# Kernel optimization log

Hardware: AMD Instinct MI355X
Metric: run time of the kernel (lower is better)

The kernel has to match this reference:

```python
import jax, jax.numpy as jnp
import numpy as np

B, L, D = 2, 2048, 768
HID = 32           # saliency gate hidden dim
WINDOWS = (8, 32)  # sorted window sizes
CLAMP_MIN, CLAMP_MAX = 0.05, 0.95
SCALE = 1.0 / np.sqrt(D)  # memory_dim == d_model


def setup_inputs() -> dict:
    key = jax.random.key(0)
    ks = jax.random.split(key, 16)
    s = 0.02
    return {
        "hidden_states": jax.random.normal(ks[0], (B, L, D), jnp.float32),
        "saliency_scores": jax.random.uniform(ks[1], (B, L), jnp.float32),
        # SaliencyGate MLP: Linear(1->HID), SiLU, Linear(HID->D)
        "gw1": jax.random.normal(ks[2], (HID, 1), jnp.float32) * s,
        "gb1": jnp.zeros((HID,), jnp.float32),
        "gw2": jax.random.normal(ks[3], (D, HID), jnp.float32) * s,
        "gb2": jnp.zeros((D,), jnp.float32),
        # SelectiveMemory projections
        "wq": jax.random.normal(ks[4], (D, D), jnp.float32) * s,
        "bq": jnp.zeros((D,), jnp.float32),
        "wk": jax.random.normal(ks[5], (D, D), jnp.float32) * s,
        "bk": jnp.zeros((D,), jnp.float32),
        "wv": jax.random.normal(ks[6], (D, D), jnp.float32) * s,
        "bv": jnp.zeros((D,), jnp.float32),
        "wo": jax.random.normal(ks[7], (D, D), jnp.float32) * s,
        "bo": jnp.zeros((D,), jnp.float32),
    }


def _forward(hidden_states, saliency_scores, gw1, gb1, gw2, gb2,
             wq, bq, wk, bk, wv, bv, wo, bo):
    # ---- SaliencyGate: scalar score -> MLP -> sigmoid gate -> clamp ----
    s = saliency_scores[..., None]                          # (b, l, 1)
    h1 = jax.nn.silu(s @ gw1.T + gb1)                       # (b, l, HID)
    gates = jax.nn.sigmoid(h1 @ gw2.T + gb2)                # (b, l, D)
    gates = jnp.clip(gates, CLAMP_MIN, CLAMP_MAX)
    h = hidden_states * gates

    # ---- SelectiveMemory: multi-window local attention ----
    q = h @ wq.T + bq                                       # (b, l, D)
    k = h @ wk.T + bk
    v = h @ wv.T + bv
    # Torch pads hidden_states with zeros before k/v projection; linear of a
    # zero row equals the bias, so padded key/value rows are exactly bk / bv.
    contexts = []
    for w in WINDOWS:
        kp = jnp.concatenate(
            [jnp.broadcast_to(bk, (B, w - 1, D)), k], axis=1)  # (b, l+w-1, D)
        vp = jnp.concatenate(
            [jnp.broadcast_to(bv, (B, w - 1, D)), v], axis=1)
        idx = jnp.arange(L)[:, None] + jnp.arange(w)[None, :]  # (l, w)
        kw = kp[:, idx]                                        # (b, l, w, D)
        vw = vp[:, idx]
        scores = jnp.einsum('bld,blwd->blw', q, kw) * SCALE
        attn = jax.nn.softmax(scores, axis=-1)
        contexts.append(jnp.einsum('blw,blwd->bld', attn, vw))
    merged = (contexts[0] + contexts[1]) * 0.5 if len(contexts) > 1 else contexts[0]
    return h + merged @ wo.T + bo


def reference(hidden_states, saliency_scores, gw1, gb1, gw2, gb2,
              wq, bq, wk, bk, wv, bv, wo, bo):
    return _forward(hidden_states, saliency_scores, gw1, gb1, gw2, gb2,
                    wq, bq, wk, bk, wv, bv, wo, bo)
```

## Files before the change

### kernel.cpp

```cpp
#include <hip/hip_runtime.h>
#include <hip/hip_bf16.h>
#include <stdint.h>

#define Bb 2
#define Ll 2048
#define Dd 768
#define HID 32
#define BL (Bb*Ll)
#define KPAD 32
#define KROWS (KPAD+Ll+16)

typedef __hip_bfloat16 bf16;
typedef __attribute__((ext_vector_type(8))) short short8;
typedef __attribute__((ext_vector_type(4))) short short4s;
typedef __attribute__((ext_vector_type(4))) float floatx4;

__device__ __forceinline__ float b2f(short u) {
    union { float f; unsigned i; } x; x.i = ((unsigned)(unsigned short)u) << 16; return x.f;
}
__device__ __forceinline__ bf16 f2b(float x) { return __float2bfloat16(x); }
__device__ __forceinline__ short f2bs(float x) {
    bf16 t = __float2bfloat16(x);
    union { bf16 h; short s; } u; u.h = t; return u.s;
}

typedef __attribute__((address_space(1))) const unsigned int guint;
typedef __attribute__((address_space(3))) unsigned int luint;
__device__ __forceinline__ void gload16(const bf16* g, bf16* l) {
    __builtin_amdgcn_global_load_lds((guint*)g, (luint*)l, 16, 0, 0);
}

#define CONV_VB 2304
#define KP_VB   (Bb*48)
#define VT_VB   ((Bb*Dd*48)/256)
#define PREP_VB (CONV_VB+KP_VB+VT_VB)
#define GATE_VB (BL/8)
__global__ __launch_bounds__(256) void prep_gate_kernel(
        const float* __restrict__ wq, const float* __restrict__ wk,
        const float* __restrict__ wv, const float* __restrict__ wo,
        const float* __restrict__ bk, const float* __restrict__ bv,
        const float* __restrict__ hidden, const float* __restrict__ sal,
        const float* __restrict__ gw1, const float* __restrict__ gb1,
        const float* __restrict__ gw2, const float* __restrict__ gb2,
        bf16* __restrict__ wout, bf16* __restrict__ kp, bf16* __restrict__ vT,
        bf16* __restrict__ h_b) {
    __shared__ bf16 g2t[32 * 770];
    __shared__ float h1s[8][HID];
    int bx = blockIdx.x, tid = threadIdx.x;
    if (bx < CONV_VB) {
        int idx = bx * 256 + tid;
        const int per = Dd * Dd / 4;
        int w = idx / per, r = idx % per;
        const float* src = (w == 0) ? wq : (w == 1) ? wk : (w == 2) ? wv : wo;
        float4 v = reinterpret_cast<const float4*>(src)[r];
        bf16* o = wout + (size_t)w * Dd * Dd + (size_t)r * 4;
        o[0] = f2b(v.x); o[1] = f2b(v.y); o[2] = f2b(v.z); o[3] = f2b(v.w);
    } else if (bx < CONV_VB + KP_VB) {
        int pb = bx - CONV_VB;
        int b = pb / 48, c = pb % 48;
        int row = (c < 32) ? c : (KPAD + Ll + (c - 32));
        size_t base = ((size_t)b * KROWS + row) * Dd;
        for (int i = tid; i < Dd; i += 256)
            kp[base + i] = (c < 32) ? f2b(bk[i]) : f2b(0.f);
    } else if (bx < PREP_VB) {
        int o = (bx - CONV_VB - KP_VB) * 256 + tid;
        int b = o / (Dd * 48); int rem = o - b * Dd * 48;
        int n = rem / 48, c = rem % 48;
        int col = (c < 32) ? c : (KPAD + Ll + (c - 32));
        vT[((size_t)b * Dd + n) * KROWS + col] = (c < 32) ? f2b(bv[n]) : f2b(0.f);
    } else {
        int row0 = (bx - PREP_VB) * 8;
#pragma unroll
        for (int k2 = 0; k2 < 24; ++k2) {
            int o4 = tid + k2 * 256;
            float4 v = reinterpret_cast<const float4*>(gw2)[o4];
            int d = o4 >> 3, j = (o4 & 7) * 4;
            g2t[(j + 0) * 770 + d] = f2b(v.x);
            g2t[(j + 1) * 770 + d] = f2b(v.y);
            g2t[(j + 2) * 770 + d] = f2b(v.z);
            g2t[(j + 3) * 770 + d] = f2b(v.w);
        }
        {
            int rr = tid >> 5, j = tid & 31;
            float s = sal[row0 + rr];
            float x = s * gw1[j] + gb1[j];
            h1s[rr][j] = x / (1.f + __expf(-x));
        }
        __syncthreads();
#pragma unroll
        for (int dl = 0; dl < 3; ++dl) {
            int d = tid + dl * 256;
            float base = gb2[d];
            float acc[8];
#pragma unroll
            for (int rr = 0; rr < 8; ++rr) acc[rr] = base;
#pragma unroll
            for (int j = 0; j < HID; ++j) {
                float wj = b2f(*(const short*)&g2t[j * 770 + d]);
#pragma unroll
                for (int rr = 0; rr < 8; ++rr) acc[rr] += h1s[rr][j] * wj;
            }
#pragma unroll
            for (int rr = 0; rr < 8; ++rr) {
                float g = 1.f / (1.f + __expf(-acc[rr]));
                g = fminf(fmaxf(g, 0.05f), 0.95f);
                size_t off = (size_t)(row0 + rr) * Dd + d;
                h_b[off] = f2b(hidden[off] * g);
            }
        }
    }
}

template<int NF, int BK>
__device__ __forceinline__ void gemm_core(const bf16* __restrict__ Ag, const bf16* __restrict__ Wg,
                                          int m0, int n0, bf16* As, bf16* Bs,
                                          floatx4 (&acc)[4][NF]) {
    const int tid  = threadIdx.x;
    const int wave = tid >> 6, lane = tid & 63;
    const int lrow = lane & 15, koff = (lane >> 4) * 8;
    const int wm = (wave >> 1) * 64, wn = (wave & 1) * (NF * 16);
    const int RS = BK * 2;
    const char* Asb = (const char*)As;
    const char* Bsb = (const char*)Bs;

    for (int k0 = 0; k0 < Dd; k0 += BK) {
#pragma unroll
        for (int c = 0; c < BK / 16; ++c) {
            int p = tid * 16 + c * 4096;
            int r = p / RS;
            int o = (p % RS) ^ ((r & 7) << 4);
            gload16(Ag + (size_t)(m0 + r) * Dd + k0 + (o >> 1),
                    As + (wave * 1024 + c * 4096) / 2);
        }
#pragma unroll
        for (int c = 0; c < NF * BK / 64; ++c) {
            int p = tid * 16 + c * 4096;
            int r = p / RS;
            int o = (p % RS) ^ ((r & 7) << 4);
            gload16(Wg + (size_t)(n0 + r) * Dd + k0 + (o >> 1),
                    Bs + (wave * 1024 + c * 4096) / 2);
        }
        __syncthreads();
#pragma unroll
        for (int kk = 0; kk < BK; kk += 32) {
            short8 a[4], b[NF];
#pragma unroll
            for (int i = 0; i < 4; ++i) {
                int row = wm + i * 16 + lrow;
                int byt = row * RS + (((kk + koff) * 2) ^ ((row & 7) << 4));
                a[i] = *reinterpret_cast<const short8*>(Asb + byt);
            }
#pragma unroll
            for (int j = 0; j < NF; ++j) {
                int row = wn + j * 16 + lrow;
                int byt = row * RS + (((kk + koff) * 2) ^ ((row & 7) << 4));
                b[j] = *reinterpret_cast<const short8*>(Bsb + byt);
            }
#pragma unroll
            for (int i = 0; i < 4; ++i)
#pragma unroll
                for (int j = 0; j < NF; ++j)
                    acc[i][j] = __builtin_amdgcn_mfma_f32_16x16x32_bf16(a[i], b[j], acc[i][j], 0, 0, 0);
        }
        __syncthreads();
    }
}

__global__ __launch_bounds__(256, 2) void gemm_qkv(
        const bf16* __restrict__ A, const bf16* __restrict__ W3,
        const float* __restrict__ bq, const float* __restrict__ bk, const float* __restrict__ bv,
        bf16* __restrict__ qo, bf16* __restrict__ kp, bf16* __restrict__ vT) {
    __shared__ bf16 As[128 * 128];
    __shared__ bf16 Bs[128 * 128];
    int bid = blockIdx.x;
    int xcd = bid & 7, idx = bid >> 3;
    int mtile = (xcd >> 1) * 8 + (idx & 7);
    int ntile = (xcd & 1) * 9 + (idx >> 3);
    int tgt = ntile / 6;
    int n0 = (ntile % 6) * 128;
    int m0 = mtile * 128;
    const bf16* W = W3 + (size_t)tgt * Dd * Dd;
    const float* bias = (tgt == 0) ? bq : (tgt == 1) ? bk : bv;

    floatx4 acc[4][4] = {};
    gemm_core<4, 128>(A, W, m0, n0, As, Bs, acc);

    int wave = threadIdx.x >> 6, lane = threadIdx.x & 63;
    int wm = (wave >> 1) * 64, wn = (wave & 1) * 64;
    int crow = (lane >> 4) * 4, ccol = lane & 15;
#pragma unroll
    for (int i = 0; i < 4; ++i)
#pragma unroll
        for (int j = 0; j < 4; ++j) {
            int n = n0 + wn + j * 16 + ccol;
            float bb = bias[n];
            int m = m0 + wm + i * 16 + crow;
            int b_ = m >> 11, l = m & 2047;
            if (tgt == 2) {
                short4s pk;
#pragma unroll
                for (int rr = 0; rr < 4; ++rr) pk[rr] = f2bs(acc[i][j][rr] + bb);
                *reinterpret_cast<short4s*>(vT + ((size_t)b_ * Dd + n) * KROWS + KPAD + l) = pk;
            } else {
#pragma unroll
                for (int rr = 0; rr < 4; ++rr) {
                    size_t orow = (tgt == 0) ? (size_t)(m + rr)
                                             : ((size_t)b_ * KROWS + KPAD + l + rr);
                    bf16* outp = (tgt == 0) ? qo : kp;
                    outp[orow * Dd + n] = f2b(acc[i][j][rr] + bb);
                }
            }
        }
}

__global__ __launch_bounds__(256, 2) void gemm_out(
        const bf16* __restrict__ A, const bf16* __restrict__ W,
        const float* __restrict__ bias, const bf16* __restrict__ addend,
        float* __restrict__ out) {
    __shared__ bf16 As[128 * 64];
    __shared__ bf16 Bs[64 * 64];
    int bid = blockIdx.x;
    int xcd = bid & 7, idx = bid >> 3;
    int mtile = (xcd >> 1) * 8 + (idx & 7);
    int ntile = (xcd & 1) * 6 + (idx >> 3);
    int n0 = ntile * 64, m0 = mtile * 128;

    floatx4 acc[4][2] = {};
    gemm_core<2, 64>(A, W, m0, n0, As, Bs, acc);

    int wave = threadIdx.x >> 6, lane = threadIdx.x & 63;
    int wm = (wave >> 1) * 64, wn = (wave & 1) * 32;
    int crow = (lane >> 4) * 4, ccol = lane & 15;
#pragma unroll
    for (int i = 0; i < 4; ++i)
#pragma unroll
        for (int j = 0; j < 2; ++j) {
            int n = n0 + wn + j * 16 + ccol;
            float bb = bias[n];
#pragma unroll
            for (int rr = 0; rr < 4; ++rr) {
                int m = m0 + wm + i * 16 + crow + rr;
                size_t o = (size_t)m * Dd + n;
                out[o] = acc[i][j][rr] + bb + b2f(*(const short*)(addend + o));
            }
        }
}

#define AW 8
__global__ __launch_bounds__(512) void attn_kernel(
        const bf16* __restrict__ q, const bf16* __restrict__ kp, const bf16* __restrict__ vT,
        bf16* __restrict__ merged) {
    __shared__ float Sp[AW][16][66];
    __shared__ bf16 wlds[AW][16 * 64];
    const int tid = threadIdx.x;
    const int wv = tid >> 6, lane = tid & 63;
    const int bid = blockIdx.x;
    const int g = (bid & 7) * 32 + (bid >> 3);
    const int b = g >> 7, L0 = (g & 127) * 16;
    const int lrow = lane & 15, koff = (lane >> 4) * 8;
    const int crow = (lane >> 4) * 4, ccol = lane & 15;
    const float scale = 0.03608439182435161f;

    const bf16* qbase = q  + ((size_t)(b * Ll + L0 + lrow)) * Dd + koff + wv * 96;
    const bf16* kbase = kp + ((size_t)b * KROWS + L0 + lrow) * Dd + koff + wv * 96;
    floatx4 s4[4] = {};
#pragma unroll
    for (int ks = 0; ks < 3; ++ks) {
        short8 a = *reinterpret_cast<const short8*>(qbase + ks * 32);
#pragma unroll
        for (int f = 0; f < 4; ++f) {
            short8 bb = *reinterpret_cast<const short8*>(kbase + (size_t)f * 16 * Dd + ks * 32);
            s4[f] = __builtin_amdgcn_mfma_f32_16x16x32_bf16(a, bb, s4[f], 0, 0, 0);
        }
    }
#pragma unroll
    for (int f = 0; f < 4; ++f)
#pragma unroll
        for (int rr = 0; rr < 4; ++rr)
            Sp[wv][crow + rr][f * 16 + ccol] = s4[f][rr];
    __syncthreads();

#pragma unroll
    for (int rr = 0; rr < 4; ++rr) {
        int r = crow + rr;
        float z[4], e[4];
#pragma unroll
        for (int f = 0; f < 4; ++f) {
            int j = f * 16 + ccol;
            float v = 0.f;
#pragma unroll
            for (int w = 0; w < AW; ++w) v += Sp[w][r][j];
            bool valid = (j >= r + 1) && (j <= r + 32);
            z[f] = valid ? v * scale : -3.0e38f;
        }
        float m = fmaxf(fmaxf(z[0], z[1]), fmaxf(z[2], z[3]));
#pragma unroll
        for (int off = 1; off < 16; off <<= 1) m = fmaxf(m, __shfl_xor(m, off));
        float S32 = 0.f, S8 = 0.f;
#pragma unroll
        for (int f = 0; f < 4; ++f) {
            e[f] = __expf(z[f] - m);
            S32 += e[f];
            int j = f * 16 + ccol;
            S8 += ((j >= r + 25) && (j <= r + 32)) ? e[f] : 0.f;
        }
#pragma unroll
        for (int off = 1; off < 16; off <<= 1) {
            S32 += __shfl_xor(S32, off);
            S8  += __shfl_xor(S8, off);
        }
        float i32 = 0.5f / S32, i8 = 0.5f / S8;
#pragma unroll
        for (int f = 0; f < 4; ++f) {
            int j = f * 16 + ccol;
            float wgt = e[f] * i32 + (((j >= r + 25) && (j <= r + 32)) ? e[f] * i8 : 0.f);
            int byt = ((r * 64 + j) * 2) ^ ((r & 7) << 4);
            *reinterpret_cast<bf16*>(reinterpret_cast<char*>(wlds[wv]) + byt) = f2b(wgt);
        }
    }

    short8 wa[2];
#pragma unroll
    for (int ks = 0; ks < 2; ++ks) {
        int byt = ((lrow * 64 + ks * 32 + koff) * 2) ^ ((lrow & 7) << 4);
        wa[ks] = *reinterpret_cast<const short8*>(reinterpret_cast<const char*>(wlds[wv]) + byt);
    }
    const bf16* vbase = vT + (size_t)b * Dd * KROWS + L0;
    bf16* obase = merged + ((size_t)(b * Ll + L0 + ccol)) * Dd;
#pragma unroll
    for (int fn = 0; fn < 6; ++fn) {
        int nr = wv * 96 + fn * 16;
        floatx4 acc = {};
#pragma unroll
        for (int ks = 0; ks < 2; ++ks) {
            short8 bb = *reinterpret_cast<const short8*>(vbase + (size_t)(nr + lrow) * KROWS + ks * 32 + koff);
            acc = __builtin_amdgcn_mfma_f32_16x16x32_bf16(bb, wa[ks], acc, 0, 0, 0);
        }
        short4s pk;
#pragma unroll
        for (int rr = 0; rr < 4; ++rr) pk[rr] = f2bs(acc[rr]);
        *reinterpret_cast<short4s*>(obase + nr + crow) = pk;
    }
}

extern "C" void kernel_launch(void* const* d_in, const int* in_sizes, int n_in,
                              void* d_out, int out_size, void* d_ws, size_t ws_size,
                              hipStream_t stream) {
    const float* hidden = (const float*)d_in[0];
    const float* sal    = (const float*)d_in[1];
    const float* gw1    = (const float*)d_in[2];
    const float* gb1    = (const float*)d_in[3];
    const float* gw2    = (const float*)d_in[4];
    const float* gb2    = (const float*)d_in[5];
    const float* wq     = (const float*)d_in[6];
    const float* bq     = (const float*)d_in[7];
    const float* wk     = (const float*)d_in[8];
    const float* bk     = (const float*)d_in[9];
    const float* wv     = (const float*)d_in[10];
    const float* bv     = (const float*)d_in[11];
    const float* wo     = (const float*)d_in[12];
    const float* bo     = (const float*)d_in[13];
    float* out = (float*)d_out;

    const size_t nBL  = (size_t)BL * Dd;
    const size_t nPad = (size_t)Bb * KROWS * Dd;
    char* p = (char*)d_ws;
    bf16* h_b = (bf16*)p; p += nBL * 2;
    bf16* q_b = (bf16*)p; p += nBL * 2;
    bf16* kpd = (bf16*)p; p += nPad * 2;
    bf16* vT  = (bf16*)p; p += nPad * 2;
    bf16* m_b = (bf16*)p; p += nBL * 2;
    bf16* w_b = (bf16*)p; p += (size_t)4 * Dd * Dd * 2;

    prep_gate_kernel<<<dim3(PREP_VB + GATE_VB), 256, 0, stream>>>(
        wq, wk, wv, wo, bk, bv, hidden, sal, gw1, gb1, gw2, gb2, w_b, kpd, vT, h_b);
    gemm_qkv<<<dim3(576), 256, 0, stream>>>(h_b, w_b, bq, bk, bv, q_b, kpd, vT);
    attn_kernel<<<dim3(256), 512, 0, stream>>>(q_b, kpd, vT, m_b);
    gemm_out<<<dim3(384), 256, 0, stream>>>(m_b, w_b + (size_t)3 * Dd * Dd, bo, h_b, out);
}
```

Before: 76.86 us.

## Double-buffer GEMM LDS tiles with BK=64 to overlap loads and MFMA

```diff
diff --git a/kernel.cpp b/kernel.cpp
--- a/kernel.cpp
+++ b/kernel.cpp
@@ -111,7 +111,7 @@
     }
 }
 
-template<int NF, int BK>
+template<int NF>
 __device__ __forceinline__ void gemm_core(const bf16* __restrict__ Ag, const bf16* __restrict__ Wg,
                                           int m0, int n0, bf16* As, bf16* Bs,
                                           floatx4 (&acc)[4][NF]) {
@@ -119,42 +119,50 @@
     const int wave = tid >> 6, lane = tid & 63;
     const int lrow = lane & 15, koff = (lane >> 4) * 8;
     const int wm = (wave >> 1) * 64, wn = (wave & 1) * (NF * 16);
-    const int RS = BK * 2;
     const char* Asb = (const char*)As;
     const char* Bsb = (const char*)Bs;
 
-    for (int k0 = 0; k0 < Dd; k0 += BK) {
-#pragma unroll
-        for (int c = 0; c < BK / 16; ++c) {
+    auto stage = [&](int buf, int k0) {
+#pragma unroll
+        for (int c = 0; c < 4; ++c) {
             int p = tid * 16 + c * 4096;
-            int r = p / RS;
-            int o = (p % RS) ^ ((r & 7) << 4);
+            int r = p >> 7;
+            int o = (p & 127) ^ ((r & 7) << 4);
             gload16(Ag + (size_t)(m0 + r) * Dd + k0 + (o >> 1),
-                    As + (wave * 1024 + c * 4096) / 2);
-        }
-#pragma unroll
-        for (int c = 0; c < NF * BK / 64; ++c) {
+                    As + buf * 8192 + (wave * 1024 + c * 4096) / 2);
+        }
+#pragma unroll
+        for (int c = 0; c < NF; ++c) {
             int p = tid * 16 + c * 4096;
-            int r = p / RS;
-            int o = (p % RS) ^ ((r & 7) << 4);
+            int r = p >> 7;
+            int o = (p & 127) ^ ((r & 7) << 4);
             gload16(Wg + (size_t)(n0 + r) * Dd + k0 + (o >> 1),
-                    Bs + (wave * 1024 + c * 4096) / 2);
-        }
-        __syncthreads();
-#pragma unroll
-        for (int kk = 0; kk < BK; kk += 32) {
+                    Bs + buf * (NF * 2048) + (wave * 1024 + c * 4096) / 2);
+        }
+    };
+
+    stage(0, 0);
+    __syncthreads();
+    int cur = 0;
+    const int NS = Dd / 64;
+    for (int step = 0; step < NS; ++step) {
+        if (step + 1 < NS) stage(cur ^ 1, (step + 1) * 64);
+        const char* Abuf = Asb + cur * 16384;
+        const char* Bbuf = Bsb + cur * (NF * 4096);
+#pragma unroll
+        for (int kk = 0; kk < 64; kk += 32) {
             short8 a[4], b[NF];
 #pragma unroll
             for (int i = 0; i < 4; ++i) {
                 int row = wm + i * 16 + lrow;
-                int byt = row * RS + (((kk + koff) * 2) ^ ((row & 7) << 4));
-                a[i] = *reinterpret_cast<const short8*>(Asb + byt);
+                int byt = (row << 7) + (((kk + koff) * 2) ^ ((row & 7) << 4));
+                a[i] = *reinterpret_cast<const short8*>(Abuf + byt);
             }
 #pragma unroll
             for (int j = 0; j < NF; ++j) {
                 int row = wn + j * 16 + lrow;
-                int byt = row * RS + (((kk + koff) * 2) ^ ((row & 7) << 4));
-                b[j] = *reinterpret_cast<const short8*>(Bsb + byt);
+                int byt = (row << 7) + (((kk + koff) * 2) ^ ((row & 7) << 4));
+                b[j] = *reinterpret_cast<const short8*>(Bbuf + byt);
             }
 #pragma unroll
             for (int i = 0; i < 4; ++i)
@@ -163,6 +171,7 @@
                     acc[i][j] = __builtin_amdgcn_mfma_f32_16x16x32_bf16(a[i], b[j], acc[i][j], 0, 0, 0);
         }
         __syncthreads();
+        cur ^= 1;
     }
 }
 
@@ -170,8 +179,8 @@
         const bf16* __restrict__ A, const bf16* __restrict__ W3,
         const float* __restrict__ bq, const float* __restrict__ bk, const float* __restrict__ bv,
         bf16* __restrict__ qo, bf16* __restrict__ kp, bf16* __restrict__ vT) {
-    __shared__ bf16 As[128 * 128];
-    __shared__ bf16 Bs[128 * 128];
+    __shared__ bf16 As[2 * 128 * 64];
+    __shared__ bf16 Bs[2 * 128 * 64];
     int bid = blockIdx.x;
     int xcd = bid & 7, idx = bid >> 3;
     int mtile = (xcd >> 1) * 8 + (idx & 7);
@@ -183,7 +192,7 @@
     const float* bias = (tgt == 0) ? bq : (tgt == 1) ? bk : bv;
 
     floatx4 acc[4][4] = {};
-    gemm_core<4, 128>(A, W, m0, n0, As, Bs, acc);
+    gemm_core<4>(A, W, m0, n0, As, Bs, acc);
 
     int wave = threadIdx.x >> 6, lane = threadIdx.x & 63;
     int wm = (wave >> 1) * 64, wn = (wave & 1) * 64;
@@ -217,8 +226,8 @@
         const bf16* __restrict__ A, const bf16* __restrict__ W,
         const float* __restrict__ bias, const bf16* __restrict__ addend,
         float* __restrict__ out) {
-    __shared__ bf16 As[128 * 64];
-    __shared__ bf16 Bs[64 * 64];
+    __shared__ bf16 As[2 * 128 * 64];
+    __shared__ bf16 Bs[2 * 64 * 64];
     int bid = blockIdx.x;
     int xcd = bid & 7, idx = bid >> 3;
     int mtile = (xcd >> 1) * 8 + (idx & 7);
@@ -226,7 +235,7 @@
     int n0 = ntile * 64, m0 = mtile * 128;
 
     floatx4 acc[4][2] = {};
-    gemm_core<2, 64>(A, W, m0, n0, As, Bs, acc);
+    gemm_core<2>(A, W, m0, n0, As, Bs, acc);
 
     int wave = threadIdx.x >> 6, lane = threadIdx.x & 63;
     int wm = (wave >> 1) * 64, wn = (wave & 1) * 32;
```

Result: no change. 78.31 us (+1.9%).
